# Kernel tuning notes

Hardware: AMD Instinct MI355X
Metric: run time of the kernel (lower is better)

The kernel has to match this reference:

```python
import jax, jax.numpy as jnp
import numpy as np

HQ, HKV, DK, DV = 8, 4, 128, 128
WIDTH, CLIP, MAXPOS = 16, 5.0, 2048
EPS = 1e-5

def rms_bn(x, g, ch_axis):
    # EMA_RMSBatchNorm (eval with batch stats): per-channel RMS over all other dims
    axes = tuple(i for i in range(x.ndim) if i != ch_axis)
    ms = jnp.mean(jnp.square(x), axis=axes, keepdims=True)
    shape = [1] * x.ndim; shape[ch_axis] = g.shape[0]
    return x * jax.lax.rsqrt(ms + EPS) * g.reshape(shape)

def ln(x, g, b):
    m = jnp.mean(x, -1, keepdims=True)
    v = jnp.mean(jnp.square(x - m), -1, keepdims=True)
    return (x - m) * jax.lax.rsqrt(v + EPS) * g + b

def rope(x):
    # x: [B,S,H,C], custom AlphaGenome frequency schedule
    B, S, H, C = x.shape
    nf = C // 2
    pos = jnp.arange(S, dtype=x.dtype)
    lin = jnp.arange(nf, dtype=x.dtype)
    end = max(MAXPOS - nf + 1.0, 1.0)
    geom = jnp.exp(jnp.linspace(0.0, np.log(end), nf).astype(x.dtype))
    inv_freq = 1.0 / (lin + geom)
    theta = jnp.repeat(pos[:, None] * inv_freq, 2, axis=-1)[None, :, None, :]  # [1,S,1,C]
    x_rot = jnp.stack([-x[..., 1::2], x[..., ::2]], axis=-1).reshape(x.shape)
    return x * jnp.cos(theta) + x_rot * jnp.sin(theta)

def _forward(x, pair_x, ab_bn_g, ab_fc_w, bn1_g, wq, wk, wv, qn_g, qn_b, kn_g, kn_b,
             vn_g, vn_b, wo, bo, bn2_g, mbn1_g, w1, b1, w2, b2, mbn2_g):
    B, S, C = x.shape
    # --- AttentionBias from pair representation ---
    pb = rms_bn(pair_x, ab_bn_g, 3)
    pb = jax.nn.gelu(pb, approximate=False)
    pb = jnp.einsum('bijc,gc->bijg', pb, ab_fc_w)          # [B,Sp,Sp,group]
    pb = jnp.repeat(jnp.repeat(pb, WIDTH, axis=1), WIDTH, axis=2)  # upsample to [B,S,S,group]
    bias = jnp.repeat(jnp.transpose(pb, (0, 3, 1, 2)), HKV, axis=1)  # [B,HQ,S,S]
    # --- GQA attention ---
    xn = rms_bn(x, bn1_g, 2)
    q = ln((xn @ wq.T).reshape(B, S, HQ, DK), qn_g, qn_b)
    k = ln((xn @ wk.T).reshape(B, S, HKV, DK), kn_g, kn_b)
    v = ln((xn @ wv.T).reshape(B, S, HKV, DV), vn_g, vn_b)
    q = rope(q); k = rope(k)
    rep = HQ // HKV
    k = jnp.tile(k, (1, 1, rep, 1))  # torch .repeat: [k0..k3, k0..k3]
    v = jnp.tile(v, (1, 1, rep, 1))
    logits = jnp.einsum('bshd,bThd->bhsT', q, k) / np.float32(np.sqrt(DK)) + bias
    logits = jnp.tanh(logits / CLIP) * CLIP
    attn = jax.nn.softmax(logits, axis=-1)
    y = jnp.einsum('bhsT,bThd->bshd', attn, v)
    # faithful to original: permute then reshape (layout scramble preserved)
    y = jnp.transpose(y, (0, 2, 1, 3)).reshape(B, S, HQ * DV)
    x = x + rms_bn(y @ wo.T + bo, bn2_g, 2)
    # --- MLP block ---
    h = jax.nn.relu(rms_bn(x, mbn1_g, 2) @ w1.T + b1)
    x = x + rms_bn(h @ w2.T + b2, mbn2_g, 2)
    return x, pair_x

def setup_inputs() -> dict:
    key = jax.random.key(0)
    ks = jax.random.split(key, 10)
    B, S, C, SP, PC = 2, 2048, 768, 128, 128
    n = lambda k, sh: jax.random.normal(k, sh, jnp.float32) * 0.02
    d = {}
    d['x'] = jax.random.normal(ks[0], (B, S, C), jnp.float32)
    d['pair_x'] = jax.random.normal(ks[1], (B, SP, SP, PC), jnp.float32)
    d['ab_bn_g'] = jnp.ones((PC,), jnp.float32)
    d['ab_fc_w'] = n(ks[2], (HQ // HKV, PC))
    d['bn1_g'] = jnp.ones((C,), jnp.float32)
    d['wq'] = n(ks[3], (HQ * DK, C))
    d['wk'] = n(ks[4], (HKV * DK, C))
    d['wv'] = n(ks[5], (HKV * DV, C))
    d['qn_g'] = jnp.ones((DK,), jnp.float32); d['qn_b'] = jnp.zeros((DK,), jnp.float32)
    d['kn_g'] = jnp.ones((DK,), jnp.float32); d['kn_b'] = jnp.zeros((DK,), jnp.float32)
    d['vn_g'] = jnp.ones((DV,), jnp.float32); d['vn_b'] = jnp.zeros((DV,), jnp.float32)
    d['wo'] = n(ks[6], (C, HQ * DV)); d['bo'] = jnp.zeros((C,), jnp.float32)
    d['bn2_g'] = jnp.ones((C,), jnp.float32)
    d['mbn1_g'] = jnp.ones((C,), jnp.float32)
    d['w1'] = n(ks[7], (2 * C, C)); d['b1'] = jnp.zeros((2 * C,), jnp.float32)
    d['w2'] = n(ks[8], (C, 2 * C)); d['b2'] = jnp.zeros((C,), jnp.float32)
    d['mbn2_g'] = jnp.ones((C,), jnp.float32)
    return d

def reference(x, pair_x, ab_bn_g, ab_fc_w, bn1_g, wq, wk, wv, qn_g, qn_b, kn_g, kn_b,
              vn_g, vn_b, wo, bo, bn2_g, mbn1_g, w1, b1, w2, b2, mbn2_g):
    return _forward(x, pair_x, ab_bn_g, ab_fc_w, bn1_g, wq, wk, wv, qn_g, qn_b, kn_g,
                    kn_b, vn_g, vn_b, wo, bo, bn2_g, mbn1_g, w1, b1, w2, b2, mbn2_g)
```

## Files before the change

kernel.cpp:

```cpp
#include <hip/hip_runtime.h>
#include <math.h>

#define EPS 1e-5f

typedef __attribute__((ext_vector_type(8))) short short8;
typedef __attribute__((ext_vector_type(4))) float f32x4;

namespace {

constexpr int Bn = 2, Sn = 2048, Cn = 768;
constexpr float INV_BS = 1.0f / 4096.0f;
constexpr float INV_PAIR = 1.0f / 32768.0f;
constexpr float LOG2E = 1.4426950408889634f;

__device__ __forceinline__ ushort f2bf(float f) {
  uint u = __float_as_uint(f);
  u = (u + 0x7fffu + ((u >> 16) & 1u)) >> 16;
  return (ushort)u;
}
__device__ __forceinline__ float bf2f(ushort u) {
  return __uint_as_float(((uint)u) << 16);
}
__device__ __forceinline__ uint cvt_pk_bf16(float lo, float hi) {
  uint r;
  asm("v_cvt_pk_bf16_f32 %0, %1, %2" : "=v"(r) : "v"(lo), "v"(hi));
  return r;
}
__device__ __forceinline__ void gl16(const ushort* g, ushort* l) {
  __builtin_amdgcn_global_load_lds(
      (const __attribute__((address_space(1))) unsigned int*)(unsigned long long)(size_t)g,
      (__attribute__((address_space(3))) unsigned int*)(unsigned int)(size_t)l, 16, 0, 0);
}

#define KSW(r, c) ((((r) * 128) + (c)) ^ (((r) & 7) * 8))
#define VTW(d, t) ((((d) * 64) + (t)) ^ (((d) & 7) * 8))
#define PSW2(w, q, c) ((w) * 2048 + ((((q) * 64) + (c)) ^ (((q) & 7) * 8)))

__global__ void castall_k(const float* __restrict__ wq, const float* __restrict__ wk,
                          const float* __restrict__ wv, const float* __restrict__ wo,
                          const float* __restrict__ w1, const float* __restrict__ w2,
                          ushort* __restrict__ dst) {
  int u = blockIdx.x * 256 + threadIdx.x;
  const float* src; int local;
  if (u < 98304)       { src = wq; local = u; }
  else if (u < 147456) { src = wk; local = u - 98304; }
  else if (u < 196608) { src = wv; local = u - 147456; }
  else if (u < 294912) { src = wo; local = u - 196608; }
  else if (u < 442368) { src = w1; local = u - 294912; }
  else                 { src = w2; local = u - 442368; }
  int i = local * 8;
  float4 a = *(const float4*)&src[i];
  float4 b = *(const float4*)&src[i + 4];
  union { short8 s8; ushort us[8]; } o;
  o.us[0] = f2bf(a.x); o.us[1] = f2bf(a.y); o.us[2] = f2bf(a.z); o.us[3] = f2bf(a.w);
  o.us[4] = f2bf(b.x); o.us[5] = f2bf(b.y); o.us[6] = f2bf(b.z); o.us[7] = f2bf(b.w);
  *(short8*)&dst[u * 8] = o.s8;
}

__global__ void rope_tab_k(float2* __restrict__ tab) {
  int idx = blockIdx.x * 256 + threadIdx.x;
  int s = idx >> 6, i = idx & 63;
  const float kGeo = logf(1985.0f) * (1.0f / 63.0f);
  float inv = 1.0f / ((float)i + expf((float)i * kGeo));
  float th = (float)s * inv;
  tab[idx] = make_float2(cosf(th), sinf(th));
}

__global__ void scale_cast_k(const float* __restrict__ a, const float* __restrict__ sums,
                             const float* __restrict__ g, ushort* __restrict__ o) {
  int idx = blockIdx.x * 256 + threadIdx.x;
  int c0 = (idx % 96) * 8;
  int base = idx * 8;
  float4 v0 = *(const float4*)&a[base];
  float4 v1 = *(const float4*)&a[base + 4];
  union { short8 s8; ushort us[8]; } r;
  float vv[8] = {v0.x, v0.y, v0.z, v0.w, v1.x, v1.y, v1.z, v1.w};
#pragma unroll
  for (int j = 0; j < 8; ++j) {
    float sc = rsqrtf(sums[c0 + j] * INV_BS + EPS) * g[c0 + j];
    r.us[j] = f2bf(vv[j] * sc);
  }
  *(short8*)&o[base] = r.s8;
}

__global__ void pair_sumsq_k(const float* __restrict__ p, float* __restrict__ out) {
  int r0 = blockIdx.x * 128;
  float acc = 0.f;
  for (int r = 0; r < 128; ++r) {
    float v = p[(size_t)(r0 + r) * 128 + threadIdx.x];
    acc += v * v;
  }
  atomicAdd(&out[threadIdx.x], acc);
}

__global__ void ch_sumsq768_k(const float* __restrict__ a, float* __restrict__ out) {
  int r0 = blockIdx.x * 16;
  int c = threadIdx.x;
  float acc = 0.f;
  for (int r = 0; r < 16; ++r) {
    float v = a[(size_t)(r0 + r) * 768 + c];
    acc += v * v;
  }
  atomicAdd(&out[c], acc);
}

__global__ void pair_bias_k(const float* __restrict__ p, const float* __restrict__ ps,
                            const float* __restrict__ g, const float* __restrict__ w,
                            float* __restrict__ pb2) {
  int idx = blockIdx.x * 128 + threadIdx.x;
  const float* row = p + (size_t)idx * 128;
  float a0 = 0.f, a1 = 0.f;
  for (int c = 0; c < 128; ++c) {
    float sc = rsqrtf(ps[c] * INV_PAIR + EPS) * g[c];
    float v = row[c] * sc;
    float ge = 0.5f * v * (1.f + erff(v * 0.70710678118654752f));
    a0 += ge * w[c];
    a1 += ge * w[128 + c];
  }
  pb2[(size_t)idx * 2 + 0] = a0 * (0.4f * LOG2E);
  pb2[(size_t)idx * 2 + 1] = a1 * (0.4f * LOG2E);
}

template <bool RELU, bool OUT_BF16>
__global__ __launch_bounds__(256) void gemm_bf16_k(
    const ushort* __restrict__ A, const ushort* __restrict__ B,
    void* __restrict__ Cv, int M, int N, int K,
    const float* __restrict__ bias) {
  __shared__ __align__(16) ushort As[128 * 64];
  __shared__ __align__(16) ushort Bs[128 * 64];
  const int m0 = blockIdx.y * 128, n0 = blockIdx.x * 128;
  const int tid = threadIdx.x;
  const int lane = tid & 63;
  const int wid = tid >> 6;
  const int l15 = lane & 15, l4 = lane >> 4;
  const int wm = (wid >> 1) * 64, wn = (wid & 1) * 64;
  const ushort* asrc[4]; const ushort* bsrc[4];
  ushort* adst[4]; ushort* bdst[4];
#pragma unroll
  for (int u = 0; u < 4; ++u) {
    int ci = u * 256 + tid;
    int r = ci >> 3, s = ci & 7, g = s ^ (r & 7);
    asrc[u] = A + (size_t)(m0 + r) * K + g * 8;
    bsrc[u] = B + (size_t)(n0 + r) * K + g * 8;
    adst[u] = &As[(u * 256 + wid * 64) * 8];
    bdst[u] = &Bs[(u * 256 + wid * 64) * 8];
  }
  f32x4 acc[4][4];
#pragma unroll
  for (int i = 0; i < 4; ++i)
#pragma unroll
    for (int j = 0; j < 4; ++j) acc[i][j] = (f32x4){0.f, 0.f, 0.f, 0.f};
  for (int k0 = 0; k0 < K; k0 += 64) {
#pragma unroll
    for (int u = 0; u < 4; ++u) {
      gl16(asrc[u] + k0, adst[u]);
      gl16(bsrc[u] + k0, bdst[u]);
    }
    __syncthreads();
#pragma unroll
    for (int ks = 0; ks < 2; ++ks) {
      const int sw = ((ks * 4 + l4) ^ (l15 & 7)) * 8;
      short8 af[4], bf[4];
#pragma unroll
      for (int i = 0; i < 4; ++i) af[i] = *(const short8*)&As[(wm + i * 16 + l15) * 64 + sw];
#pragma unroll
      for (int j = 0; j < 4; ++j) bf[j] = *(const short8*)&Bs[(wn + j * 16 + l15) * 64 + sw];
#pragma unroll
      for (int i = 0; i < 4; ++i)
#pragma unroll
        for (int j = 0; j < 4; ++j)
          acc[i][j] = __builtin_amdgcn_mfma_f32_16x16x32_bf16(af[i], bf[j], acc[i][j], 0, 0, 0);
    }
    __syncthreads();
  }
  float* Cf = (float*)Cv;
  ushort* Cb = (ushort*)Cv;
#pragma unroll
  for (int j = 0; j < 4; ++j) {
    int col = n0 + wn + j * 16 + l15;
    float bv = bias ? bias[col] : 0.f;
#pragma unroll
    for (int i = 0; i < 4; ++i) {
      int row = m0 + wm + i * 16 + l4 * 4;
#pragma unroll
      for (int r = 0; r < 4; ++r) {
        float v = acc[i][j][r] + bv;
        if (RELU) v = fmaxf(v, 0.f);
        if (OUT_BF16) Cb[(size_t)(row + r) * N + col] = f2bf(v);
        else Cf[(size_t)(row + r) * N + col] = v;
      }
    }
  }
}

template <bool SUMSQ>
__global__ __launch_bounds__(256) void gemm64_bf16_k(
    const ushort* __restrict__ A, const ushort* __restrict__ B,
    float* __restrict__ Cf, int M, int N, int K,
    const float* __restrict__ bias, float* __restrict__ ssq) {
  __shared__ __align__(16) ushort As[64 * 64];
  __shared__ __align__(16) ushort Bs[128 * 64];
  const int m0 = blockIdx.y * 64, n0 = blockIdx.x * 128;
  const int tid = threadIdx.x;
  const int lane = tid & 63;
  const int wid = tid >> 6;
  const int l15 = lane & 15, l4 = lane >> 4;
  const int wn = wid * 32;
  const ushort* asrc[2]; ushort* adst[2];
  const ushort* bsrc[4]; ushort* bdst[4];
#pragma unroll
  for (int u = 0; u < 2; ++u) {
    int ci = u * 256 + tid;
    int r = ci >> 3, s = ci & 7, g = s ^ (r & 7);
    asrc[u] = A + (size_t)(m0 + r) * K + g * 8;
    adst[u] = &As[(u * 256 + wid * 64) * 8];
  }
#pragma unroll
  for (int u = 0; u < 4; ++u) {
    int ci = u * 256 + tid;
    int r = ci >> 3, s = ci & 7, g = s ^ (r & 7);
    bsrc[u] = B + (size_t)(n0 + r) * K + g * 8;
    bdst[u] = &Bs[(u * 256 + wid * 64) * 8];
  }
  f32x4 acc[4][2];
#pragma unroll
  for (int i = 0; i < 4; ++i)
#pragma unroll
    for (int j = 0; j < 2; ++j) acc[i][j] = (f32x4){0.f, 0.f, 0.f, 0.f};
  for (int k0 = 0; k0 < K; k0 += 64) {
#pragma unroll
    for (int u = 0; u < 2; ++u) gl16(asrc[u] + k0, adst[u]);
#pragma unroll
    for (int u = 0; u < 4; ++u) gl16(bsrc[u] + k0, bdst[u]);
    __syncthreads();
#pragma unroll
    for (int ks = 0; ks < 2; ++ks) {
      const int sw = ((ks * 4 + l4) ^ (l15 & 7)) * 8;
      short8 af[4], bf[2];
#pragma unroll
      for (int i = 0; i < 4; ++i) af[i] = *(const short8*)&As[(i * 16 + l15) * 64 + sw];
#pragma unroll
      for (int j = 0; j < 2; ++j) bf[j] = *(const short8*)&Bs[(wn + j * 16 + l15) * 64 + sw];
#pragma unroll
      for (int i = 0; i < 4; ++i)
#pragma unroll
        for (int j = 0; j < 2; ++j)
          acc[i][j] = __builtin_amdgcn_mfma_f32_16x16x32_bf16(af[i], bf[j], acc[i][j], 0, 0, 0);
    }
    __syncthreads();
  }
#pragma unroll
  for (int j = 0; j < 2; ++j) {
    int col = n0 + wn + j * 16 + l15;
    float bv = bias ? bias[col] : 0.f;
    float sq = 0.f;
#pragma unroll
    for (int i = 0; i < 4; ++i) {
      int row = m0 + i * 16 + l4 * 4;
#pragma unroll
      for (int r = 0; r < 4; ++r) {
        float v = acc[i][j][r] + bv;
        if (SUMSQ) sq += v * v;
        Cf[(size_t)(row + r) * N + col] = v;
      }
    }
    if (SUMSQ) {
      sq += __shfl_xor(sq, 16);
      sq += __shfl_xor(sq, 32);
      if (l4 == 0) atomicAdd(&ssq[col], sq);
    }
  }
}

__global__ __launch_bounds__(256) void ln_rope_k(
    const float* __restrict__ qkv, const float2* __restrict__ rtab,
    const float* __restrict__ qg, const float* __restrict__ qb,
    const float* __restrict__ kg, const float* __restrict__ kb,
    const float* __restrict__ vg, const float* __restrict__ vb,
    ushort* __restrict__ q_b, ushort* __restrict__ k_b, ushort* __restrict__ v_b) {
  const int half = threadIdx.x >> 7;
  const int tid = threadIdx.x & 127;
  const int bs = blockIdx.x * 2 + half;
  const int slot = blockIdx.y;
  const int s = bs & (Sn - 1);
  const int b = bs >> 11;
  const float* src; const float* g; const float* be; ushort* dst; bool dorope; bool isq = false;
  if (slot < 8) {
    src = qkv + (size_t)bs * 2048 + slot * 128;
    g = qg; be = qb;
    dst = q_b + ((size_t)(b * 8 + slot) * Sn + s) * 128;
    dorope = true; isq = true;
  } else if (slot < 12) {
    int h = slot - 8;
    src = qkv + (size_t)bs * 2048 + 1024 + h * 128;
    g = kg; be = kb;
    dst = k_b + ((size_t)(b * 4 + h) * Sn + s) * 128;
    dorope = true;
  } else {
    int h = slot - 12;
    src = qkv + (size_t)bs * 2048 + 1536 + h * 128;
    g = vg; be = vb;
    dst = v_b + ((size_t)(b * 4 + h) * Sn + s) * 128;
    dorope = false;
  }
  __shared__ float sh[2][128];
  __shared__ float red[2][4];
  float v = src[tid];
  float sum = v;
#pragma unroll
  for (int o = 32; o >= 1; o >>= 1) sum += __shfl_xor(sum, o);
  if ((tid & 63) == 0) red[half][tid >> 6] = sum;
  __syncthreads();
  float mean = (red[half][0] + red[half][1]) * (1.f / 128.f);
  float d = v - mean;
  float s2 = d * d;
#pragma unroll
  for (int o = 32; o >= 1; o >>= 1) s2 += __shfl_xor(s2, o);
  if ((tid & 63) == 0) red[half][2 + (tid >> 6)] = s2;
  __syncthreads();
  float var = (red[half][2] + red[half][3]) * (1.f / 128.f);
  float val = d * rsqrtf(var + EPS) * g[tid] + be[tid];
  if (dorope) {
    sh[half][tid] = val;
    __syncthreads();
    float2 cssn = rtab[(s << 6) | (tid >> 1)];
    float rot = (tid & 1) ? sh[half][tid - 1] : -sh[half][tid + 1];
    val = val * cssn.x + rot * cssn.y;
  }
  if (isq) val *= 0.035355339059327376f * LOG2E;
  dst[tid] = f2bf(val);
}

__global__ __launch_bounds__(256) void vtrans_k(const ushort* __restrict__ vb,
                                                ushort* __restrict__ vtt) {
  __shared__ __align__(16) ushort T[64][136];
  const int hv = blockIdx.y, s0 = blockIdx.x * 64;
  const int tid = threadIdx.x;
  const ushort* src = vb + ((size_t)hv * Sn + s0) * 128;
#pragma unroll
  for (int u = 0; u < 4; ++u) {
    int fi = u * 256 + tid;
    int r = fi >> 4, c = (fi & 15) * 8;
    *(float4*)&T[r][c] = *(const float4*)&src[(size_t)r * 128 + c];
  }
  __syncthreads();
  ushort* dst = vtt + (size_t)hv * 128 * Sn + s0;
#pragma unroll
  for (int u = 0; u < 4; ++u) {
    int fi = u * 256 + tid;
    int d = fi >> 3, t8 = (fi & 7) * 8;
    union { float4 f4; ushort us[8]; } o;
#pragma unroll
    for (int j = 0; j < 8; ++j) o.us[j] = T[t8 + j][d];
    *(float4*)&dst[(size_t)d * Sn + t8] = o.f4;
  }
}

__global__ __launch_bounds__(256, 2) void flash_v11_k(
    const ushort* __restrict__ qb, const ushort* __restrict__ kb,
    const ushort* __restrict__ vtt, const float* __restrict__ pb2,
    ushort* __restrict__ part_y, float* __restrict__ part_l) {
  __shared__ __align__(16) ushort Ks[64 * 128];
  __shared__ __align__(16) ushort Vt[128 * 64];
  const int s0 = blockIdx.x * 128;
  const int bh = blockIdx.y;
  const int half = blockIdx.z;
  const int b = bh >> 3, h = bh & 7;
  const int kv = h & 3, grp = h >> 2;
  const int tid = threadIdx.x;
  const int wid = tid >> 6, lane = tid & 63;
  const int l15 = lane & 15, l4 = lane >> 4;
  const ushort* kbase = kb + (size_t)(b * 4 + kv) * Sn * 128;
  const ushort* vbase = vtt + (size_t)(b * 4 + kv) * 128 * Sn;
  const int qr0 = s0 + wid * 32;
  short8 qf[2][4];
#pragma unroll
  for (int rg = 0; rg < 2; ++rg)
#pragma unroll
    for (int kc = 0; kc < 4; ++kc)
      qf[rg][kc] = *(const short8*)&qb[((size_t)bh * Sn + qr0 + rg * 16 + l15) * 128 + kc * 32 + l4 * 8];
  const ushort* ksrc[4]; const ushort* vsrc[4];
  ushort* kdst[4]; ushort* vdst[4];
#pragma unroll
  for (int u = 0; u < 4; ++u) {
    int ci = u * 256 + tid;
    int kr = ci >> 4, kg = (ci & 15) ^ (kr & 7);
    ksrc[u] = kbase + (size_t)kr * 128 + kg * 8;
    kdst[u] = &Ks[(u * 256 + wid * 64) * 8];
    int vd = ci >> 3, vg = (ci & 7) ^ (vd & 7);
    vsrc[u] = vbase + (size_t)vd * Sn + vg * 8;
    vdst[u] = &Vt[(u * 256 + wid * 64) * 8];
  }
  f32x4 y[2][8];
#pragma unroll
  for (int rg = 0; rg < 2; ++rg)
#pragma unroll
    for (int i = 0; i < 8; ++i) y[rg][i] = (f32x4){0.f, 0.f, 0.f, 0.f};
  float lsum[2] = {0.f, 0.f};
  const float C2 = -10.f * LOG2E;
  const int tbeg = half * 512;
  for (int t0 = tbeg; t0 < tbeg + 512; t0 += 64) {
    __syncthreads();
#pragma unroll
    for (int u = 0; u < 4; ++u) {
      gl16(ksrc[u] + (size_t)t0 * 128, kdst[u]);
      gl16(vsrc[u] + t0, vdst[u]);
    }
    __syncthreads();
    f32x4 acc[2][4];
#pragma unroll
    for (int rg = 0; rg < 2; ++rg)
#pragma unroll
      for (int nb = 0; nb < 4; ++nb) acc[rg][nb] = (f32x4){0.f, 0.f, 0.f, 0.f};
    __builtin_amdgcn_s_setprio(1);
#pragma unroll
    for (int kc = 0; kc < 4; ++kc)
#pragma unroll
      for (int nb = 0; nb < 4; ++nb) {
        short8 kf = *(const short8*)&Ks[KSW(nb * 16 + l15, kc * 32 + l4 * 8)];
        acc[0][nb] = __builtin_amdgcn_mfma_f32_16x16x32_bf16(kf, qf[0][kc], acc[0][nb], 0, 0, 0);
        acc[1][nb] = __builtin_amdgcn_mfma_f32_16x16x32_bf16(kf, qf[1][kc], acc[1][nb], 0, 0, 0);
      }
    __builtin_amdgcn_s_setprio(0);
    __syncthreads();
#pragma unroll
    for (int rg = 0; rg < 2; ++rg)
#pragma unroll
      for (int nb = 0; nb < 4; ++nb) {
        float bias = pb2[(((size_t)b * 128 + (s0 >> 4) + wid * 2 + rg) * 128 + (t0 >> 4) + nb) * 2 + grp];
        float p[4];
#pragma unroll
        for (int r = 0; r < 4; ++r) {
          float e = exp2f(acc[rg][nb][r] + bias);
          p[r] = exp2f(C2 * __builtin_amdgcn_rcpf(e + 1.f));
        }
        lsum[rg] += (p[0] + p[1]) + (p[2] + p[3]);
        uint2 pk;
        pk.x = cvt_pk_bf16(p[0], p[1]);
        pk.y = cvt_pk_bf16(p[2], p[3]);
        *(uint2*)&Ks[PSW2(wid, rg * 16 + l15, nb * 16 + l4 * 4)] = pk;
      }
    __builtin_amdgcn_s_setprio(1);
#pragma unroll
    for (int ks = 0; ks < 2; ++ks) {
      short8 pa0 = *(const short8*)&Ks[PSW2(wid, l15, ks * 32 + l4 * 8)];
      short8 pa1 = *(const short8*)&Ks[PSW2(wid, 16 + l15, ks * 32 + l4 * 8)];
#pragma unroll
      for (int nbd = 0; nbd < 8; ++nbd) {
        short8 vf = *(const short8*)&Vt[VTW(nbd * 16 + l15, ks * 32 + l4 * 8)];
        y[0][nbd] = __builtin_amdgcn_mfma_f32_16x16x32_bf16(pa0, vf, y[0][nbd], 0, 0, 0);
        y[1][nbd] = __builtin_amdgcn_mfma_f32_16x16x32_bf16(pa1, vf, y[1][nbd], 0, 0, 0);
      }
    }
    __builtin_amdgcn_s_setprio(0);
  }
#pragma unroll
  for (int rg = 0; rg < 2; ++rg) {
    float ls = lsum[rg];
    ls += __shfl_xor(ls, 16);
    ls += __shfl_xor(ls, 32);
    if (l4 == 0) part_l[(size_t)(half * 16 + bh) * Sn + qr0 + rg * 16 + l15] = ls;
    ushort* pybase = part_y + ((size_t)(half * 16 + bh) * Sn + qr0 + rg * 16) * 128;
#pragma unroll
    for (int nbd = 0; nbd < 8; ++nbd)
#pragma unroll
      for (int r = 0; r < 4; ++r)
        pybase[(size_t)(l4 * 4 + r) * 128 + nbd * 16 + l15] = f2bf(y[rg][nbd][r]);
  }
}

__global__ void combine_k(const ushort* __restrict__ part_y, const float* __restrict__ part_l,
                          ushort* __restrict__ attn_b) {
  int t = blockIdx.x * 256 + threadIdx.x;
  int row = t >> 4;
  size_t o0 = (size_t)row * 128 + (t & 15) * 8;
  float acc[8] = {};
#pragma unroll
  for (int hf = 0; hf < 4; ++hf) {
    union { short8 s8; ushort us[8]; } u;
    u.s8 = *(const short8*)&part_y[o0 + (size_t)hf * 4194304];
#pragma unroll
    for (int j = 0; j < 8; ++j) acc[j] += bf2f(u.us[j]);
  }
  float rcp = 1.f / (part_l[row] + part_l[row + 32768] + part_l[row + 65536] + part_l[row + 98304]);
  union { short8 s8; ushort us[8]; } o;
#pragma unroll
  for (int j = 0; j < 8; ++j) o.us[j] = f2bf(acc[j] * rcp);
  *(short8*)&attn_b[o0] = o.s8;
}

template <bool SUMSQ>
__global__ void add_scale_k(const float* __restrict__ base, const float* __restrict__ delta,
                            const float* __restrict__ sums, const float* __restrict__ g,
                            float* __restrict__ out, float* __restrict__ ssq) {
  const int c = threadIdx.x;
  const float sc = rsqrtf(sums[c] * INV_BS + EPS) * g[c];
  const int r0 = blockIdx.x * 16;
  float sq = 0.f;
  for (int r = 0; r < 16; ++r) {
    size_t idx = (size_t)(r0 + r) * 768 + c;
    float v = base[idx] + delta[idx] * sc;
    out[idx] = v;
    if (SUMSQ) sq += v * v;
  }
  if (SUMSQ) atomicAdd(&ssq[c], sq);
}

}

extern "C" void kernel_launch(void* const* d_in, const int* in_sizes, int n_in,
                              void* d_out, int out_size, void* d_ws, size_t ws_size,
                              hipStream_t stream) {
  const float* x       = (const float*)d_in[0];
  const float* pair_x  = (const float*)d_in[1];
  const float* ab_bn_g = (const float*)d_in[2];
  const float* ab_fc_w = (const float*)d_in[3];
  const float* bn1_g   = (const float*)d_in[4];
  const float* wq      = (const float*)d_in[5];
  const float* wk      = (const float*)d_in[6];
  const float* wv      = (const float*)d_in[7];
  const float* qn_g    = (const float*)d_in[8];
  const float* qn_b    = (const float*)d_in[9];
  const float* kn_g    = (const float*)d_in[10];
  const float* kn_b    = (const float*)d_in[11];
  const float* vn_g    = (const float*)d_in[12];
  const float* vn_b    = (const float*)d_in[13];
  const float* wo      = (const float*)d_in[14];
  const float* bo      = (const float*)d_in[15];
  const float* bn2_g   = (const float*)d_in[16];
  const float* mbn1_g  = (const float*)d_in[17];
  const float* w1      = (const float*)d_in[18];
  const float* b1      = (const float*)d_in[19];
  const float* w2      = (const float*)d_in[20];
  const float* b2      = (const float*)d_in[21];
  const float* mbn2_g  = (const float*)d_in[22];
  float* out = (float*)d_out;
  float* ws = (float*)d_ws;

  float* ps    = ws + 0;
  float* xs    = ws + 256;
  float* es    = ws + 1024;
  float* x2s   = ws + 2048;
  float* fs    = ws + 3072;
  float* pb2   = ws + 4096;
  ushort* wall_b = (ushort*)(ws + 69632);
  ushort* wo_b = (ushort*)(ws + 856064);
  ushort* w1_b = (ushort*)(ws + 1249280);
  ushort* w2_b = (ushort*)(ws + 1839104);
  ushort* xn_b = (ushort*)(ws + 2428928);
  float* qkvtmp = ws + 4001792;
  ushort* q_b  = (ushort*)(ws + 12390400);
  ushort* k_b  = (ushort*)(ws + 14487552);
  ushort* v_b  = (ushort*)(ws + 15536128);
  float2* rtab = (float2*)(ws + 16584704);
  ushort* v_tt = (ushort*)(ws + 2428928);
  ushort* part_y = (ushort*)(ws + 3477504);
  float* part_l = ws + 11866112;
  ushort* attn_b = (ushort*)(ws + 11997184);
  float* proj  = ws + 3477504;
  float* x2    = ws + 6623232;
  ushort* x2n_b = (ushort*)(ws + 9768960);
  ushort* hbuf_b = (ushort*)(ws + 3477504);
  float* proj2 = ws + 11341824;

  (void)hipMemsetAsync(ws, 0, 4096 * sizeof(float), stream);

  castall_k<<<2304, 256, 0, stream>>>(wq, wk, wv, wo, w1, w2, wall_b);
  rope_tab_k<<<512, 256, 0, stream>>>(rtab);

  pair_sumsq_k<<<256, 128, 0, stream>>>(pair_x, ps);
  pair_bias_k<<<256, 128, 0, stream>>>(pair_x, ps, ab_bn_g, ab_fc_w, pb2);
  ch_sumsq768_k<<<256, 768, 0, stream>>>(x, xs);
  scale_cast_k<<<1536, 256, 0, stream>>>(x, xs, bn1_g, xn_b);
  gemm_bf16_k<false, false><<<dim3(16, 32), 256, 0, stream>>>(xn_b, wall_b, qkvtmp, 4096, 2048, 768, nullptr);
  ln_rope_k<<<dim3(2048, 16), 256, 0, stream>>>(qkvtmp, rtab, qn_g, qn_b, kn_g, kn_b,
                                                vn_g, vn_b, q_b, k_b, v_b);
  vtrans_k<<<dim3(32, 8), 256, 0, stream>>>(v_b, v_tt);
  flash_v11_k<<<dim3(16, 16, 4), 256, 0, stream>>>(q_b, k_b, v_tt, pb2, part_y, part_l);
  combine_k<<<2048, 256, 0, stream>>>(part_y, part_l, attn_b);
  gemm64_bf16_k<true><<<dim3(6, 64), 256, 0, stream>>>(attn_b, wo_b, proj, 4096, 768, 1024, bo, es);
  add_scale_k<true><<<256, 768, 0, stream>>>(x, proj, es, bn2_g, x2, x2s);
  scale_cast_k<<<1536, 256, 0, stream>>>(x2, x2s, mbn1_g, x2n_b);
  gemm_bf16_k<true, true><<<dim3(12, 32), 256, 0, stream>>>(x2n_b, w1_b, hbuf_b, 4096, 1536, 768, b1);
  gemm64_bf16_k<true><<<dim3(6, 64), 256, 0, stream>>>(hbuf_b, w2_b, proj2, 4096, 768, 1536, b2, fs);
  add_scale_k<false><<<256, 768, 0, stream>>>(x2, proj2, fs, mbn2_g, out, nullptr);

  (void)hipMemcpyAsync(out + 3145728, pair_x, (size_t)4194304 * sizeof(float),
                       hipMemcpyDeviceToDevice, stream);
}
```

Measured before the change: 295.0 us.

## Fuse pair passthrough copy into pair-bias kernel and split P buffer in flash

The pair-bias kernel is rewritten so 32 lanes share each row with float4 loads and a shuffle reduction. The same kernel now writes the pair_x passthrough copy into the output, so the separate device-to-device memcpy of 16 MB goes away. The flash kernel stages P in a dedicated shared-memory buffer instead of reusing the K tile, which lets one __syncthreads per iteration be dropped. The cost is extra LDS per block, which may limit occupancy.

```diff
diff --git a/kernel.cpp b/kernel.cpp
--- a/kernel.cpp
+++ b/kernel.cpp
@@ -104,21 +104,48 @@
   atomicAdd(&out[c], acc);
 }
 
-__global__ void pair_bias_k(const float* __restrict__ p, const float* __restrict__ ps,
-                            const float* __restrict__ g, const float* __restrict__ w,
-                            float* __restrict__ pb2) {
-  int idx = blockIdx.x * 128 + threadIdx.x;
-  const float* row = p + (size_t)idx * 128;
-  float a0 = 0.f, a1 = 0.f;
-  for (int c = 0; c < 128; ++c) {
-    float sc = rsqrtf(ps[c] * INV_PAIR + EPS) * g[c];
-    float v = row[c] * sc;
-    float ge = 0.5f * v * (1.f + erff(v * 0.70710678118654752f));
-    a0 += ge * w[c];
-    a1 += ge * w[128 + c];
-  }
-  pb2[(size_t)idx * 2 + 0] = a0 * (0.4f * LOG2E);
-  pb2[(size_t)idx * 2 + 1] = a1 * (0.4f * LOG2E);
+__global__ __launch_bounds__(256) void pair_bias_k(
+    const float* __restrict__ p, const float* __restrict__ ps,
+    const float* __restrict__ g, const float* __restrict__ w,
+    float* __restrict__ pb2, float* __restrict__ pcopy) {
+  const int tid = threadIdx.x;
+  const int lane32 = tid & 31;
+  const int sub = tid >> 5;
+  const int c0 = lane32 * 4;
+  float4 gv = *(const float4*)&g[c0];
+  float4 psv = *(const float4*)&ps[c0];
+  float4 w0 = *(const float4*)&w[c0];
+  float4 w1v = *(const float4*)&w[128 + c0];
+  float sc[4] = {rsqrtf(psv.x * INV_PAIR + EPS) * gv.x,
+                 rsqrtf(psv.y * INV_PAIR + EPS) * gv.y,
+                 rsqrtf(psv.z * INV_PAIR + EPS) * gv.z,
+                 rsqrtf(psv.w * INV_PAIR + EPS) * gv.w};
+  float wa[4] = {w0.x, w0.y, w0.z, w0.w};
+  float wb[4] = {w1v.x, w1v.y, w1v.z, w1v.w};
+#pragma unroll
+  for (int it = 0; it < 4; ++it) {
+    int row = blockIdx.x * 32 + it * 8 + sub;
+    float4 v = *(const float4*)&p[(size_t)row * 128 + c0];
+    *(float4*)&pcopy[(size_t)row * 128 + c0] = v;
+    float vv[4] = {v.x, v.y, v.z, v.w};
+    float a0 = 0.f, a1 = 0.f;
+#pragma unroll
+    for (int j = 0; j < 4; ++j) {
+      float x = vv[j] * sc[j];
+      float ge = 0.5f * x * (1.f + erff(x * 0.70710678118654752f));
+      a0 += ge * wa[j];
+      a1 += ge * wb[j];
+    }
+#pragma unroll
+    for (int o = 1; o <= 16; o <<= 1) {
+      a0 += __shfl_xor(a0, o);
+      a1 += __shfl_xor(a1, o);
+    }
+    if (lane32 == 0) {
+      pb2[(size_t)row * 2 + 0] = a0 * (0.4f * LOG2E);
+      pb2[(size_t)row * 2 + 1] = a1 * (0.4f * LOG2E);
+    }
+  }
 }
 
 template <bool RELU, bool OUT_BF16>
@@ -356,12 +383,13 @@
   }
 }
 
-__global__ __launch_bounds__(256, 2) void flash_v11_k(
+__global__ __launch_bounds__(256, 2) void flash_v13_k(
     const ushort* __restrict__ qb, const ushort* __restrict__ kb,
     const ushort* __restrict__ vtt, const float* __restrict__ pb2,
     ushort* __restrict__ part_y, float* __restrict__ part_l) {
   __shared__ __align__(16) ushort Ks[64 * 128];
   __shared__ __align__(16) ushort Vt[128 * 64];
+  __shared__ __align__(16) ushort Ps[4 * 32 * 64];
   const int s0 = blockIdx.x * 128;
   const int bh = blockIdx.y;
   const int half = blockIdx.z;
@@ -422,7 +450,6 @@
         acc[1][nb] = __builtin_amdgcn_mfma_f32_16x16x32_bf16(kf, qf[1][kc], acc[1][nb], 0, 0, 0);
       }
     __builtin_amdgcn_s_setprio(0);
-    __syncthreads();
 #pragma unroll
     for (int rg = 0; rg < 2; ++rg)
 #pragma unroll
@@ -438,13 +465,13 @@
         uint2 pk;
         pk.x = cvt_pk_bf16(p[0], p[1]);
         pk.y = cvt_pk_bf16(p[2], p[3]);
-        *(uint2*)&Ks[PSW2(wid, rg * 16 + l15, nb * 16 + l4 * 4)] = pk;
+        *(uint2*)&Ps[PSW2(wid, rg * 16 + l15, nb * 16 + l4 * 4)] = pk;
       }
     __builtin_amdgcn_s_setprio(1);
 #pragma unroll
     for (int ks = 0; ks < 2; ++ks) {
-      short8 pa0 = *(const short8*)&Ks[PSW2(wid, l15, ks * 32 + l4 * 8)];
-      short8 pa1 = *(const short8*)&Ks[PSW2(wid, 16 + l15, ks * 32 + l4 * 8)];
+      short8 pa0 = *(const short8*)&Ps[PSW2(wid, l15, ks * 32 + l4 * 8)];
+      short8 pa1 = *(const short8*)&Ps[PSW2(wid, 16 + l15, ks * 32 + l4 * 8)];
 #pragma unroll
       for (int nbd = 0; nbd < 8; ++nbd) {
         short8 vf = *(const short8*)&Vt[VTW(nbd * 16 + l15, ks * 32 + l4 * 8)];
@@ -569,14 +596,14 @@
   rope_tab_k<<<512, 256, 0, stream>>>(rtab);
 
   pair_sumsq_k<<<256, 128, 0, stream>>>(pair_x, ps);
-  pair_bias_k<<<256, 128, 0, stream>>>(pair_x, ps, ab_bn_g, ab_fc_w, pb2);
+  pair_bias_k<<<1024, 256, 0, stream>>>(pair_x, ps, ab_bn_g, ab_fc_w, pb2, out + 3145728);
   ch_sumsq768_k<<<256, 768, 0, stream>>>(x, xs);
   scale_cast_k<<<1536, 256, 0, stream>>>(x, xs, bn1_g, xn_b);
   gemm_bf16_k<false, false><<<dim3(16, 32), 256, 0, stream>>>(xn_b, wall_b, qkvtmp, 4096, 2048, 768, nullptr);
   ln_rope_k<<<dim3(2048, 16), 256, 0, stream>>>(qkvtmp, rtab, qn_g, qn_b, kn_g, kn_b,
                                                 vn_g, vn_b, q_b, k_b, v_b);
   vtrans_k<<<dim3(32, 8), 256, 0, stream>>>(v_b, v_tt);
-  flash_v11_k<<<dim3(16, 16, 4), 256, 0, stream>>>(q_b, k_b, v_tt, pb2, part_y, part_l);
+  flash_v13_k<<<dim3(16, 16, 4), 256, 0, stream>>>(q_b, k_b, v_tt, pb2, part_y, part_l);
   combine_k<<<2048, 256, 0, stream>>>(part_y, part_l, attn_b);
   gemm64_bf16_k<true><<<dim3(6, 64), 256, 0, stream>>>(attn_b, wo_b, proj, 4096, 768, 1024, bo, es);
   add_scale_k<true><<<256, 768, 0, stream>>>(x, proj, es, bn2_g, x2, x2s);
@@ -584,7 +611,4 @@
   gemm_bf16_k<true, true><<<dim3(12, 32), 256, 0, stream>>>(x2n_b, w1_b, hbuf_b, 4096, 1536, 768, b1);
   gemm64_bf16_k<true><<<dim3(6, 64), 256, 0, stream>>>(hbuf_b, w2_b, proj2, 4096, 768, 1536, b2, fs);
   add_scale_k<false><<<256, 768, 0, stream>>>(x2, proj2, fs, mbn2_g, out, nullptr);
-
-  (void)hipMemcpyAsync(out + 3145728, pair_x, (size_t)4194304 * sizeof(float),
-                       hipMemcpyDeviceToDevice, stream);
-}
+}
```

Measured after the change: 266.7 us. 9.6% less time.
